# Kernel optimization log

Measured on AMD Instinct MI355X. Metric: run time of the kernel, lower is better.

Reference implementation:

```python
import jax, jax.numpy as jnp
import numpy as np

N_NODES = 100000
N_EDGES = 1600000
D = 128


def setup_inputs() -> dict:
    key = jax.random.key(0)
    ks = jax.random.split(key, 10)
    features = jax.random.normal(ks[0], (N_NODES, D), dtype=jnp.float32)
    edge_index = jax.random.randint(ks[1], (2, N_EDGES), 0, N_NODES, dtype=jnp.int64)
    edge_weight = jax.random.uniform(ks[2], (N_EDGES,), dtype=jnp.float32)
    scale = 1.0 / np.sqrt(D)
    W1 = jax.random.normal(ks[3], (D, D), dtype=jnp.float32) * scale
    b1 = jnp.zeros((D,), dtype=jnp.float32)
    a1 = jnp.full((D,), 0.25, dtype=jnp.float32)  # PReLU init
    W2 = jax.random.normal(ks[4], (D, D), dtype=jnp.float32) * scale
    b2 = jnp.zeros((D,), dtype=jnp.float32)
    a2 = jnp.full((D,), 0.25, dtype=jnp.float32)
    return {"features": features, "edge_index": edge_index, "edge_weight": edge_weight,
            "W1": W1, "b1": b1, "a1": a1, "W2": W2, "b2": b2, "a2": a2}


def _gcn_norm(edge_index, edge_weight, n_nodes):
    # PyG GCNConv default: add self-loops (weight 1), symmetric normalization.
    src, dst = edge_index[0], edge_index[1]
    loop = jnp.arange(n_nodes, dtype=src.dtype)
    src = jnp.concatenate([src, loop])
    dst = jnp.concatenate([dst, loop])
    w = jnp.concatenate([edge_weight, jnp.ones((n_nodes,), edge_weight.dtype)])
    deg = jax.ops.segment_sum(w, dst, num_segments=n_nodes)  # in-degree (target)
    dis = jnp.where(deg > 0, jax.lax.rsqrt(deg), 0.0)
    norm = dis[src] * w * dis[dst]  # [E + N]
    return src, dst, norm


def _gcn_layer(x, W, b, src, dst, norm, n_nodes):
    h = x @ W                                 # [N, D] dense GEMM first (PyG order)
    msg = h[src] * norm[:, None]              # gather + scale, [E+N, D]
    out = jax.ops.segment_sum(msg, dst, num_segments=n_nodes)
    return out + b


def _prelu(x, a):
    return jnp.where(x >= 0, x, a * x)


def reference(features, edge_index, edge_weight, W1, b1, a1, W2, b2, a2):
    n = features.shape[0]
    src, dst, norm = _gcn_norm(edge_index, edge_weight, n)
    # dropout is identity in eval mode
    x = _prelu(_gcn_layer(features, W1, b1, src, dst, norm, n), a1)
    x = _prelu(_gcn_layer(x, W2, b2, src, dst, norm, n), a2)
    return x
```

## Files before the change

### kernel.cpp

```cpp
#include <hip/hip_runtime.h>
#include <cstdint>

#define NN 100000
#define NE 1600000
#define DD 128
#define NB 250
#define BSZ 400
#define NHB ((NE + 8191) / 8192)

typedef unsigned int uint;
typedef unsigned short ushort;
typedef unsigned long long u64;

typedef __attribute__((ext_vector_type(8))) short short8;
typedef __attribute__((ext_vector_type(4))) float floatx4;

__device__ inline uint f2bf(float f) {
    uint u = __float_as_uint(f);
    return (u + 0x7fffu + ((u >> 16) & 1u)) >> 16;
}


__global__ __launch_bounds__(256) void bucket_hist(const int* __restrict__ dst,
                                                   uint* __restrict__ bcp) {
    __shared__ uint h[NB];
    int tid = threadIdx.x;
    if (tid < NB) h[tid] = 0u;
    __syncthreads();
    int e0 = blockIdx.x * 8192 + tid;
#pragma unroll
    for (int k = 0; k < 32; ++k) {
        int e = e0 + 256 * k;
        if (e < NE) atomicAdd(&h[(uint)dst[e] / BSZ], 1u);
    }
    __syncthreads();
    if (tid < NB) bcp[blockIdx.x * 256 + tid] = h[tid];
}

__global__ __launch_bounds__(256) void bucket_prefix(const uint* __restrict__ bcp,
                                                     uint* __restrict__ bbase,
                                                     uint* __restrict__ bcur) {
    __shared__ uint cnt[NB];
    int tid = threadIdx.x;
    if (tid < NB) {
        uint s = 0;
        for (int j = 0; j < NHB; ++j) s += bcp[j * 256 + tid];
        cnt[tid] = s;
    }
    __syncthreads();
    int lane = tid;
    if (lane < 64) {
        uint v[4], s = 0;
#pragma unroll
        for (int k = 0; k < 4; ++k) {
            int i = lane * 4 + k;
            v[k] = (i < NB) ? cnt[i] : 0u;
            s += v[k];
        }
        uint inc = s;
#pragma unroll
        for (int d = 1; d < 64; d <<= 1) {
            uint t = __shfl_up(inc, (unsigned)d, 64);
            if (lane >= d) inc += t;
        }
        uint run = inc - s;
#pragma unroll
        for (int k = 0; k < 4; ++k) {
            int i = lane * 4 + k;
            if (i < NB) { bbase[i] = run; bcur[i] = run; run += v[k]; }
        }
        if (lane == 63) bbase[NB] = run;
    }
}

__global__ __launch_bounds__(256) void bucket_append(const int* __restrict__ src,
                                                     const int* __restrict__ dst,
                                                     const float* __restrict__ w,
                                                     uint* __restrict__ bcur,
                                                     int2* __restrict__ etmp) {
    __shared__ uint h[NB];
    __shared__ uint res[NB];
    int tid = threadIdx.x;
    if (tid < NB) h[tid] = 0u;
    __syncthreads();
    int e0 = blockIdx.x * 4096 + tid;
    uint rank[16], bkt[16];
#pragma unroll
    for (int k = 0; k < 16; ++k) {
        int e = e0 + 256 * k;
        if (e < NE) {
            uint b = (uint)dst[e] / BSZ;
            bkt[k] = b;
            rank[k] = atomicAdd(&h[b], 1u);
        } else bkt[k] = 0xffffffffu;
    }
    __syncthreads();
    if (tid < NB) res[tid] = h[tid] ? atomicAdd(&bcur[tid], h[tid]) : 0u;
    __syncthreads();
#pragma unroll
    for (int k = 0; k < 16; ++k) {
        if (bkt[k] != 0xffffffffu) {
            int e = e0 + 256 * k;
            uint dl = (uint)dst[e] - bkt[k] * BSZ;
            uint wq = (uint)(w[e] * 8388608.0f);
            if (wq > 8388607u) wq = 8388607u;
            etmp[res[bkt[k]] + rank[k]] = make_int2(src[e], (int)((dl << 23) | wq));
        }
    }
}

__global__ __launch_bounds__(256) void bucket_build(const int2* __restrict__ etmp,
                                                    const uint* __restrict__ bbase,
                                                    float* __restrict__ dis,
                                                    int* __restrict__ hist_g,
                                                    int* __restrict__ rowstart,
                                                    int2* __restrict__ edges) {
    __shared__ u64   wc[BSZ];
    __shared__ uint  cur[BSZ];
    __shared__ float disl[BSZ];
    int tid = threadIdx.x;
    int b = blockIdx.x;
    int n0 = b * BSZ;
    for (int i = tid; i < BSZ; i += 256) wc[i] = 0ull;
    __syncthreads();
    uint base = bbase[b], end = bbase[b + 1];
    for (uint i = base + tid; i < end; i += 256) {
        uint y = (uint)etmp[i].y;
        uint dl = y >> 23;
        atomicAdd(&wc[dl], ((u64)1 << 40) | (u64)(y & 0x7fffffu));
    }
    __syncthreads();
    if (tid < 64) {
        uint v[7], s = 0;
#pragma unroll
        for (int k = 0; k < 7; ++k) {
            int i = tid * 7 + k;
            v[k] = (i < BSZ) ? (uint)(wc[i] >> 40) : 0u;
            s += v[k];
        }
        uint inc = s;
#pragma unroll
        for (int d = 1; d < 64; d <<= 1) {
            uint t = __shfl_up(inc, (unsigned)d, 64);
            if (tid >= d) inc += t;
        }
        uint run = inc - s;
#pragma unroll
        for (int k = 0; k < 7; ++k) {
            int i = tid * 7 + k;
            if (i < BSZ) { cur[i] = run; run += v[k]; }
        }
    }
    __syncthreads();
    for (int i = tid; i < BSZ; i += 256) {
        u64 v = wc[i];
        float wsum = (float)(v & 0xffffffffffull) * (1.0f / 8388608.0f);
        float ds = rsqrtf(1.0f + wsum);
        disl[i] = ds;
        dis[n0 + i] = ds;
        hist_g[n0 + i] = (int)(v >> 40);
        rowstart[n0 + i] = (int)(base + cur[i]);
    }
    __syncthreads();
    for (uint i = base + tid; i < end; i += 256) {
        int2 e = etmp[i];
        uint y = (uint)e.y;
        uint dl = y >> 23;
        float wv = (float)(y & 0x7fffffu) * (1.0f / 8388608.0f);
        uint p = atomicAdd(&cur[dl], 1u);
        float nrm = wv * disl[dl];
        edges[base + p] = make_int2(e.x, __float_as_int(nrm));
    }
}

#define WTS 136
#define NTILES ((NN + 63) / 64)

template <bool AF32>
__global__ __launch_bounds__(256) void gemm_mfma(const void* __restrict__ Xv,
                                                 const float* __restrict__ W,
                                                 const float* __restrict__ dis,
                                                 ushort* __restrict__ HB) {
    __shared__ ushort Wt[DD * WTS];
    int tid = threadIdx.x;
#pragma unroll
    for (int it = 0; it < 16; ++it) {
        int flat = (tid + it * 256) * 4;
        int k = flat >> 7, n = flat & 127;
        float4 wv = *(const float4*)&W[flat];
        Wt[(n + 0) * WTS + k] = (ushort)f2bf(wv.x);
        Wt[(n + 1) * WTS + k] = (ushort)f2bf(wv.y);
        Wt[(n + 2) * WTS + k] = (ushort)f2bf(wv.z);
        Wt[(n + 3) * WTS + k] = (ushort)f2bf(wv.w);
    }
    __syncthreads();

    int wave = tid >> 6, lane = tid & 63;
    int q = lane >> 4, l16 = lane & 15;

    for (int tile = blockIdx.x; tile < NTILES; tile += gridDim.x) {
        int row0 = tile * 64 + wave * 16;

        int arow = row0 + l16;
        if (arow >= NN) arow = NN - 1;
        short8 afr[4];
        if (AF32) {
            const float* xr = (const float*)Xv + (size_t)arow * DD + q * 8;
#pragma unroll
            for (int ks = 0; ks < 4; ++ks) {
                float4 f0 = *(const float4*)(xr + ks * 32);
                float4 f1 = *(const float4*)(xr + ks * 32 + 4);
                uint4 u;
                u.x = f2bf(f0.x) | (f2bf(f0.y) << 16);
                u.y = f2bf(f0.z) | (f2bf(f0.w) << 16);
                u.z = f2bf(f1.x) | (f2bf(f1.y) << 16);
                u.w = f2bf(f1.z) | (f2bf(f1.w) << 16);
                afr[ks] = __builtin_bit_cast(short8, u);
            }
        } else {
            const ushort* xr = (const ushort*)Xv + (size_t)arow * DD + q * 8;
#pragma unroll
            for (int ks = 0; ks < 4; ++ks)
                afr[ks] = *(const short8*)(xr + ks * 32);
        }

        floatx4 acc[8];
#pragma unroll
        for (int ct = 0; ct < 8; ++ct) acc[ct] = (floatx4)(0.0f);

#pragma unroll
        for (int ct = 0; ct < 8; ++ct) {
            const ushort* wp = &Wt[(ct * 16 + l16) * WTS + q * 8];
#pragma unroll
            for (int ks = 0; ks < 4; ++ks) {
                short8 bfr = *(const short8*)(wp + ks * 32);
                acc[ct] = __builtin_amdgcn_mfma_f32_16x16x32_bf16(afr[ks], bfr, acc[ct], 0, 0, 0);
            }
        }

#pragma unroll
        for (int reg = 0; reg < 4; ++reg) {
            int r = row0 + q * 4 + reg;
            if (r < NN) {
                float ds = dis[r];
                ushort* orow = HB + (size_t)r * DD + l16;
#pragma unroll
                for (int ct = 0; ct < 8; ++ct)
                    orow[ct * 16] = (ushort)f2bf(acc[ct][reg] * ds);
            }
        }
    }
}

template <bool BF16OUT>
__global__ __launch_bounds__(256) void gather_finalize(const ushort* __restrict__ hb,
                                                       const int2* __restrict__ edges,
                                                       const int* __restrict__ rowstart,
                                                       const int* __restrict__ hist,
                                                       const float* __restrict__ dis,
                                                       const float* __restrict__ b,
                                                       const float* __restrict__ a,
                                                       void* __restrict__ xout) {
    int wid = __builtin_amdgcn_readfirstlane(threadIdx.x >> 6);
    int lane = threadIdx.x & 63;
    int nodeA = blockIdx.x * 8 + wid * 2;
    int nodeB = nodeA + 1;
    uint lane4 = (uint)lane * 4u;
    const char* hbase = (const char*)hb;

    int rsA  = rowstart[nodeA];
    int rsB  = rowstart[nodeB];
    int cntA = hist[nodeA];
    int cntB = hist[nodeB];
    float dsA = dis[nodeA];
    float dsB = dis[nodeB];
    const int2* epA = edges + rsA;
    const int2* epB = edges + rsB;

    uint suA = *(const uint*)(hbase + ((size_t)(uint)nodeA << 8) + lane4);
    uint suB = *(const uint*)(hbase + ((size_t)(uint)nodeB << 8) + lane4);
    float2 a0, a1, a2, a3, b0, b1, b2, b3;
    a0.x = __uint_as_float(suA << 16) * dsA;
    a0.y = __uint_as_float(suA & 0xffff0000u) * dsA;
    b0.x = __uint_as_float(suB << 16) * dsB;
    b0.y = __uint_as_float(suB & 0xffff0000u) * dsB;
    a1 = make_float2(0.f, 0.f); a2 = a1; a3 = a1;
    b1 = a1; b2 = a1; b3 = a1;

    int nbA = (cntA + 15) >> 4;
    int nbB = (cntB + 15) >> 4;
    int nb = nbA > nbB ? nbA : nbB;

    for (int t = 0; t < nb; ++t) {
        int remA = cntA - t * 16;
        int remB = cntB - t * 16;
        int2 eA[16], eB[16];
#pragma unroll
        for (int k = 0; k < 16; ++k) eA[k] = epA[t * 16 + k];
#pragma unroll
        for (int k = 0; k < 16; ++k) eB[k] = epB[t * 16 + k];

        uint gA[16], gB[16];
        float nA[16], nB[16];
#pragma unroll
        for (int k = 0; k < 16; ++k) {
            bool live = k < remA;
            uint s = live ? (uint)eA[k].x : 0u;
            nA[k] = live ? __int_as_float(eA[k].y) : 0.0f;
            gA[k] = *(const uint*)(hbase + ((size_t)s << 8) + lane4);
        }
#pragma unroll
        for (int k = 0; k < 16; ++k) {
            bool live = k < remB;
            uint s = live ? (uint)eB[k].x : 0u;
            nB[k] = live ? __int_as_float(eB[k].y) : 0.0f;
            gB[k] = *(const uint*)(hbase + ((size_t)s << 8) + lane4);
        }
#pragma unroll
        for (int k = 0; k < 16; ++k) {
            float2* ac = (k & 3) == 0 ? &a0 : (k & 3) == 1 ? &a1 : (k & 3) == 2 ? &a2 : &a3;
            ac->x += __uint_as_float(gA[k] << 16) * nA[k];
            ac->y += __uint_as_float(gA[k] & 0xffff0000u) * nA[k];
        }
#pragma unroll
        for (int k = 0; k < 16; ++k) {
            float2* ac = (k & 3) == 0 ? &b0 : (k & 3) == 1 ? &b1 : (k & 3) == 2 ? &b2 : &b3;
            ac->x += __uint_as_float(gB[k] << 16) * nB[k];
            ac->y += __uint_as_float(gB[k] & 0xffff0000u) * nB[k];
        }
    }

    float2 bb = ((const float2*)b)[lane];
    float2 aa = ((const float2*)a)[lane];
    float rA0 = a0.x + a1.x + a2.x + a3.x + bb.x;
    float rA1 = a0.y + a1.y + a2.y + a3.y + bb.y;
    float rB0 = b0.x + b1.x + b2.x + b3.x + bb.x;
    float rB1 = b0.y + b1.y + b2.y + b3.y + bb.y;
    rA0 = rA0 >= 0.f ? rA0 : aa.x * rA0;
    rA1 = rA1 >= 0.f ? rA1 : aa.y * rA1;
    rB0 = rB0 >= 0.f ? rB0 : aa.x * rB0;
    rB1 = rB1 >= 0.f ? rB1 : aa.y * rB1;
    if (BF16OUT) {
        ((uint*)xout)[(size_t)nodeA * 64 + lane] = f2bf(rA0) | (f2bf(rA1) << 16);
        ((uint*)xout)[(size_t)nodeB * 64 + lane] = f2bf(rB0) | (f2bf(rB1) << 16);
    } else {
        float2 oA; oA.x = rA0; oA.y = rA1;
        float2 oB; oB.x = rB0; oB.y = rB1;
        ((float2*)xout)[(size_t)nodeA * 64 + lane] = oA;
        ((float2*)xout)[(size_t)nodeB * 64 + lane] = oB;
    }
}

extern "C" void kernel_launch(void* const* d_in, const int* in_sizes, int n_in,
                              void* d_out, int out_size, void* d_ws, size_t ws_size,
                              hipStream_t stream) {
    const float* feat = (const float*)d_in[0];
    const int*   ei   = (const int*)d_in[1];
    const float* ew   = (const float*)d_in[2];
    const float* W1   = (const float*)d_in[3];
    const float* b1   = (const float*)d_in[4];
    const float* a1   = (const float*)d_in[5];
    const float* W2   = (const float*)d_in[6];
    const float* b2   = (const float*)d_in[7];
    const float* a2   = (const float*)d_in[8];
    float* out = (float*)d_out;

    const int* srcp = ei;
    const int* dstp = ei + NE;

    char* wsb = (char*)d_ws;
    size_t off = 0;
    uint* bcp    = (uint*)(wsb + off); off += 4ull * 256 * NHB;
    uint* bbase  = (uint*)(wsb + off); off += 4096;
    uint* bcur   = (uint*)(wsb + off); off += 4096;
    float* dis   = (float*)(wsb + off); off += 4ull * NN;
    int* hist    = (int*)(wsb + off); off += 4ull * NN;
    int* rowstart= (int*)(wsb + off); off += 4ull * NN;
    int2* etmp   = (int2*)(wsb + off); off += 8ull * NE;
    int2* edges  = (int2*)(wsb + off); off += 8ull * NE;
    ushort* hb   = (ushort*)(wsb + off); off += 2ull * NN * DD;
    ushort* x1b  = (ushort*)(wsb + off); off += 2ull * NN * DD;

    bucket_hist<<<NHB, 256, 0, stream>>>(dstp, bcp);
    bucket_prefix<<<1, 256, 0, stream>>>(bcp, bbase, bcur);
    bucket_append<<<(NE + 4095) / 4096, 256, 0, stream>>>(srcp, dstp, ew, bcur, etmp);
    bucket_build<<<NB, 256, 0, stream>>>(etmp, bbase, dis, hist, rowstart, edges);

    const int gemm_blocks = (NTILES + 1) / 2;
    const int gath_blocks = NN / 8;

    gemm_mfma<true><<<gemm_blocks, 256, 0, stream>>>(feat, W1, dis, hb);
    gather_finalize<true><<<gath_blocks, 256, 0, stream>>>(hb, edges, rowstart, hist, dis, b1, a1, x1b);
    gemm_mfma<false><<<gemm_blocks, 256, 0, stream>>>(x1b, W2, dis, hb);
    gather_finalize<false><<<gath_blocks, 256, 0, stream>>>(hb, edges, rowstart, hist, dis, b2, a2, out);
}
```

Measured before the change: 368.9 us.

## Fuse all stages into one persistent cooperative kernel with grid syncs

Replaces the eight separate launches (bucket histogram, prefix, append, build, two GEMMs, two gathers) with one cooperative persistent kernel that uses grid-wide syncs between phases. Weight transpose and bf16 conversion move to a first phase in global memory so GEMM blocks only copy them into LDS. The aim is to remove launch gaps and per-kernel ramp-up and tail. In exchange the grid is capped by occupancy, so the gather phase gets far fewer resident blocks than before, and grid.sync barriers add their own cost.

```diff
diff --git a/kernel.cpp b/kernel.cpp
--- a/kernel.cpp
+++ b/kernel.cpp
@@ -1,12 +1,17 @@
 #include <hip/hip_runtime.h>
+#include <hip/hip_cooperative_groups.h>
 #include <cstdint>
+
+namespace cg = cooperative_groups;
 
 #define NN 100000
 #define NE 1600000
 #define DD 128
 #define NB 250
 #define BSZ 400
-#define NHB ((NE + 8191) / 8192)
+#define GB 1024
+#define WTS 136
+#define NTILES ((NN + 63) / 64)
 
 typedef unsigned int uint;
 typedef unsigned short ushort;
@@ -14,193 +19,42 @@
 
 typedef __attribute__((ext_vector_type(8))) short short8;
 typedef __attribute__((ext_vector_type(4))) float floatx4;
+
+struct FusedP {
+    const float* feat; const int* srcp; const int* dstp; const float* ew;
+    const float* W1; const float* b1; const float* a1;
+    const float* W2; const float* b2; const float* a2;
+    ushort* wt1; ushort* wt2;
+    uint* bcp; uint* bbase; uint* bcur;
+    float* dis; int* hist; int* rowstart;
+    int2* etmp; int2* edges;
+    ushort* hb; ushort* x1b; float* out;
+};
 
 __device__ inline uint f2bf(float f) {
     uint u = __float_as_uint(f);
     return (u + 0x7fffu + ((u >> 16) & 1u)) >> 16;
 }
 
-
-__global__ __launch_bounds__(256) void bucket_hist(const int* __restrict__ dst,
-                                                   uint* __restrict__ bcp) {
-    __shared__ uint h[NB];
-    int tid = threadIdx.x;
-    if (tid < NB) h[tid] = 0u;
+template <bool AF32>
+__device__ __forceinline__ void gemm_phase(const void* Xv, const ushort* Wtg,
+                                           const float* dis, ushort* HB,
+                                           char* smem, int tid) {
+    ushort* Wt = (ushort*)smem;
+#pragma unroll
+    for (int u = 0; u < 8; ++u) {
+        int unit = tid + u * 256;
+        int n = unit >> 4, c = unit & 15;
+        *(short8*)&Wt[n * WTS + c * 8] = *(const short8*)(Wtg + n * DD + c * 8);
+    }
     __syncthreads();
-    int e0 = blockIdx.x * 8192 + tid;
-#pragma unroll
-    for (int k = 0; k < 32; ++k) {
-        int e = e0 + 256 * k;
-        if (e < NE) atomicAdd(&h[(uint)dst[e] / BSZ], 1u);
-    }
-    __syncthreads();
-    if (tid < NB) bcp[blockIdx.x * 256 + tid] = h[tid];
-}
-
-__global__ __launch_bounds__(256) void bucket_prefix(const uint* __restrict__ bcp,
-                                                     uint* __restrict__ bbase,
-                                                     uint* __restrict__ bcur) {
-    __shared__ uint cnt[NB];
-    int tid = threadIdx.x;
-    if (tid < NB) {
-        uint s = 0;
-        for (int j = 0; j < NHB; ++j) s += bcp[j * 256 + tid];
-        cnt[tid] = s;
-    }
-    __syncthreads();
-    int lane = tid;
-    if (lane < 64) {
-        uint v[4], s = 0;
-#pragma unroll
-        for (int k = 0; k < 4; ++k) {
-            int i = lane * 4 + k;
-            v[k] = (i < NB) ? cnt[i] : 0u;
-            s += v[k];
-        }
-        uint inc = s;
-#pragma unroll
-        for (int d = 1; d < 64; d <<= 1) {
-            uint t = __shfl_up(inc, (unsigned)d, 64);
-            if (lane >= d) inc += t;
-        }
-        uint run = inc - s;
-#pragma unroll
-        for (int k = 0; k < 4; ++k) {
-            int i = lane * 4 + k;
-            if (i < NB) { bbase[i] = run; bcur[i] = run; run += v[k]; }
-        }
-        if (lane == 63) bbase[NB] = run;
-    }
-}
-
-__global__ __launch_bounds__(256) void bucket_append(const int* __restrict__ src,
-                                                     const int* __restrict__ dst,
-                                                     const float* __restrict__ w,
-                                                     uint* __restrict__ bcur,
-                                                     int2* __restrict__ etmp) {
-    __shared__ uint h[NB];
-    __shared__ uint res[NB];
-    int tid = threadIdx.x;
-    if (tid < NB) h[tid] = 0u;
-    __syncthreads();
-    int e0 = blockIdx.x * 4096 + tid;
-    uint rank[16], bkt[16];
-#pragma unroll
-    for (int k = 0; k < 16; ++k) {
-        int e = e0 + 256 * k;
-        if (e < NE) {
-            uint b = (uint)dst[e] / BSZ;
-            bkt[k] = b;
-            rank[k] = atomicAdd(&h[b], 1u);
-        } else bkt[k] = 0xffffffffu;
-    }
-    __syncthreads();
-    if (tid < NB) res[tid] = h[tid] ? atomicAdd(&bcur[tid], h[tid]) : 0u;
-    __syncthreads();
-#pragma unroll
-    for (int k = 0; k < 16; ++k) {
-        if (bkt[k] != 0xffffffffu) {
-            int e = e0 + 256 * k;
-            uint dl = (uint)dst[e] - bkt[k] * BSZ;
-            uint wq = (uint)(w[e] * 8388608.0f);
-            if (wq > 8388607u) wq = 8388607u;
-            etmp[res[bkt[k]] + rank[k]] = make_int2(src[e], (int)((dl << 23) | wq));
-        }
-    }
-}
-
-__global__ __launch_bounds__(256) void bucket_build(const int2* __restrict__ etmp,
-                                                    const uint* __restrict__ bbase,
-                                                    float* __restrict__ dis,
-                                                    int* __restrict__ hist_g,
-                                                    int* __restrict__ rowstart,
-                                                    int2* __restrict__ edges) {
-    __shared__ u64   wc[BSZ];
-    __shared__ uint  cur[BSZ];
-    __shared__ float disl[BSZ];
-    int tid = threadIdx.x;
-    int b = blockIdx.x;
-    int n0 = b * BSZ;
-    for (int i = tid; i < BSZ; i += 256) wc[i] = 0ull;
-    __syncthreads();
-    uint base = bbase[b], end = bbase[b + 1];
-    for (uint i = base + tid; i < end; i += 256) {
-        uint y = (uint)etmp[i].y;
-        uint dl = y >> 23;
-        atomicAdd(&wc[dl], ((u64)1 << 40) | (u64)(y & 0x7fffffu));
-    }
-    __syncthreads();
-    if (tid < 64) {
-        uint v[7], s = 0;
-#pragma unroll
-        for (int k = 0; k < 7; ++k) {
-            int i = tid * 7 + k;
-            v[k] = (i < BSZ) ? (uint)(wc[i] >> 40) : 0u;
-            s += v[k];
-        }
-        uint inc = s;
-#pragma unroll
-        for (int d = 1; d < 64; d <<= 1) {
-            uint t = __shfl_up(inc, (unsigned)d, 64);
-            if (tid >= d) inc += t;
-        }
-        uint run = inc - s;
-#pragma unroll
-        for (int k = 0; k < 7; ++k) {
-            int i = tid * 7 + k;
-            if (i < BSZ) { cur[i] = run; run += v[k]; }
-        }
-    }
-    __syncthreads();
-    for (int i = tid; i < BSZ; i += 256) {
-        u64 v = wc[i];
-        float wsum = (float)(v & 0xffffffffffull) * (1.0f / 8388608.0f);
-        float ds = rsqrtf(1.0f + wsum);
-        disl[i] = ds;
-        dis[n0 + i] = ds;
-        hist_g[n0 + i] = (int)(v >> 40);
-        rowstart[n0 + i] = (int)(base + cur[i]);
-    }
-    __syncthreads();
-    for (uint i = base + tid; i < end; i += 256) {
-        int2 e = etmp[i];
-        uint y = (uint)e.y;
-        uint dl = y >> 23;
-        float wv = (float)(y & 0x7fffffu) * (1.0f / 8388608.0f);
-        uint p = atomicAdd(&cur[dl], 1u);
-        float nrm = wv * disl[dl];
-        edges[base + p] = make_int2(e.x, __float_as_int(nrm));
-    }
-}
-
-#define WTS 136
-#define NTILES ((NN + 63) / 64)
-
-template <bool AF32>
-__global__ __launch_bounds__(256) void gemm_mfma(const void* __restrict__ Xv,
-                                                 const float* __restrict__ W,
-                                                 const float* __restrict__ dis,
-                                                 ushort* __restrict__ HB) {
-    __shared__ ushort Wt[DD * WTS];
-    int tid = threadIdx.x;
-#pragma unroll
-    for (int it = 0; it < 16; ++it) {
-        int flat = (tid + it * 256) * 4;
-        int k = flat >> 7, n = flat & 127;
-        float4 wv = *(const float4*)&W[flat];
-        Wt[(n + 0) * WTS + k] = (ushort)f2bf(wv.x);
-        Wt[(n + 1) * WTS + k] = (ushort)f2bf(wv.y);
-        Wt[(n + 2) * WTS + k] = (ushort)f2bf(wv.z);
-        Wt[(n + 3) * WTS + k] = (ushort)f2bf(wv.w);
-    }
-    __syncthreads();
-
-    int wave = tid >> 6, lane = tid & 63;
+
+    int lane = tid & 63;
+    int wave = tid >> 6;
     int q = lane >> 4, l16 = lane & 15;
 
     for (int tile = blockIdx.x; tile < NTILES; tile += gridDim.x) {
         int row0 = tile * 64 + wave * 16;
-
         int arow = row0 + l16;
         if (arow >= NN) arow = NN - 1;
         short8 afr[4];
@@ -250,147 +104,319 @@
             }
         }
     }
+    __syncthreads();
 }
 
 template <bool BF16OUT>
-__global__ __launch_bounds__(256) void gather_finalize(const ushort* __restrict__ hb,
-                                                       const int2* __restrict__ edges,
-                                                       const int* __restrict__ rowstart,
-                                                       const int* __restrict__ hist,
-                                                       const float* __restrict__ dis,
-                                                       const float* __restrict__ b,
-                                                       const float* __restrict__ a,
-                                                       void* __restrict__ xout) {
-    int wid = __builtin_amdgcn_readfirstlane(threadIdx.x >> 6);
-    int lane = threadIdx.x & 63;
-    int nodeA = blockIdx.x * 8 + wid * 2;
-    int nodeB = nodeA + 1;
+__device__ __forceinline__ void gather_phase(const ushort* hb, const int2* edges,
+                                             const int* rowstart, const int* hist,
+                                             const float* dis, const float* bv,
+                                             const float* av, void* xout, int tid) {
+    int wid = __builtin_amdgcn_readfirstlane(tid >> 6);
+    int lane = tid & 63;
     uint lane4 = (uint)lane * 4u;
     const char* hbase = (const char*)hb;
 
-    int rsA  = rowstart[nodeA];
-    int rsB  = rowstart[nodeB];
-    int cntA = hist[nodeA];
-    int cntB = hist[nodeB];
-    float dsA = dis[nodeA];
-    float dsB = dis[nodeB];
-    const int2* epA = edges + rsA;
-    const int2* epB = edges + rsB;
-
-    uint suA = *(const uint*)(hbase + ((size_t)(uint)nodeA << 8) + lane4);
-    uint suB = *(const uint*)(hbase + ((size_t)(uint)nodeB << 8) + lane4);
-    float2 a0, a1, a2, a3, b0, b1, b2, b3;
-    a0.x = __uint_as_float(suA << 16) * dsA;
-    a0.y = __uint_as_float(suA & 0xffff0000u) * dsA;
-    b0.x = __uint_as_float(suB << 16) * dsB;
-    b0.y = __uint_as_float(suB & 0xffff0000u) * dsB;
-    a1 = make_float2(0.f, 0.f); a2 = a1; a3 = a1;
-    b1 = a1; b2 = a1; b3 = a1;
-
-    int nbA = (cntA + 15) >> 4;
-    int nbB = (cntB + 15) >> 4;
-    int nb = nbA > nbB ? nbA : nbB;
-
-    for (int t = 0; t < nb; ++t) {
-        int remA = cntA - t * 16;
-        int remB = cntB - t * 16;
-        int2 eA[16], eB[16];
-#pragma unroll
-        for (int k = 0; k < 16; ++k) eA[k] = epA[t * 16 + k];
-#pragma unroll
-        for (int k = 0; k < 16; ++k) eB[k] = epB[t * 16 + k];
-
-        uint gA[16], gB[16];
-        float nA[16], nB[16];
-#pragma unroll
-        for (int k = 0; k < 16; ++k) {
-            bool live = k < remA;
-            uint s = live ? (uint)eA[k].x : 0u;
-            nA[k] = live ? __int_as_float(eA[k].y) : 0.0f;
-            gA[k] = *(const uint*)(hbase + ((size_t)s << 8) + lane4);
-        }
-#pragma unroll
-        for (int k = 0; k < 16; ++k) {
-            bool live = k < remB;
-            uint s = live ? (uint)eB[k].x : 0u;
-            nB[k] = live ? __int_as_float(eB[k].y) : 0.0f;
-            gB[k] = *(const uint*)(hbase + ((size_t)s << 8) + lane4);
-        }
-#pragma unroll
-        for (int k = 0; k < 16; ++k) {
-            float2* ac = (k & 3) == 0 ? &a0 : (k & 3) == 1 ? &a1 : (k & 3) == 2 ? &a2 : &a3;
-            ac->x += __uint_as_float(gA[k] << 16) * nA[k];
-            ac->y += __uint_as_float(gA[k] & 0xffff0000u) * nA[k];
-        }
-#pragma unroll
-        for (int k = 0; k < 16; ++k) {
-            float2* ac = (k & 3) == 0 ? &b0 : (k & 3) == 1 ? &b1 : (k & 3) == 2 ? &b2 : &b3;
-            ac->x += __uint_as_float(gB[k] << 16) * nB[k];
-            ac->y += __uint_as_float(gB[k] & 0xffff0000u) * nB[k];
-        }
-    }
-
-    float2 bb = ((const float2*)b)[lane];
-    float2 aa = ((const float2*)a)[lane];
-    float rA0 = a0.x + a1.x + a2.x + a3.x + bb.x;
-    float rA1 = a0.y + a1.y + a2.y + a3.y + bb.y;
-    float rB0 = b0.x + b1.x + b2.x + b3.x + bb.x;
-    float rB1 = b0.y + b1.y + b2.y + b3.y + bb.y;
-    rA0 = rA0 >= 0.f ? rA0 : aa.x * rA0;
-    rA1 = rA1 >= 0.f ? rA1 : aa.y * rA1;
-    rB0 = rB0 >= 0.f ? rB0 : aa.x * rB0;
-    rB1 = rB1 >= 0.f ? rB1 : aa.y * rB1;
-    if (BF16OUT) {
-        ((uint*)xout)[(size_t)nodeA * 64 + lane] = f2bf(rA0) | (f2bf(rA1) << 16);
-        ((uint*)xout)[(size_t)nodeB * 64 + lane] = f2bf(rB0) | (f2bf(rB1) << 16);
-    } else {
-        float2 oA; oA.x = rA0; oA.y = rA1;
-        float2 oB; oB.x = rB0; oB.y = rB1;
-        ((float2*)xout)[(size_t)nodeA * 64 + lane] = oA;
-        ((float2*)xout)[(size_t)nodeB * 64 + lane] = oB;
-    }
+    for (int g = blockIdx.x; g < NN / 8; g += gridDim.x) {
+        int nodeA = g * 8 + wid * 2;
+        int nodeB = nodeA + 1;
+
+        int rsA  = rowstart[nodeA];
+        int rsB  = rowstart[nodeB];
+        int cntA = hist[nodeA];
+        int cntB = hist[nodeB];
+        float dsA = dis[nodeA];
+        float dsB = dis[nodeB];
+        const int2* epA = edges + rsA;
+        const int2* epB = edges + rsB;
+
+        uint suA = *(const uint*)(hbase + ((size_t)(uint)nodeA << 8) + lane4);
+        uint suB = *(const uint*)(hbase + ((size_t)(uint)nodeB << 8) + lane4);
+        float2 a0, a1, a2, a3, b0, b1, b2, b3;
+        a0.x = __uint_as_float(suA << 16) * dsA;
+        a0.y = __uint_as_float(suA & 0xffff0000u) * dsA;
+        b0.x = __uint_as_float(suB << 16) * dsB;
+        b0.y = __uint_as_float(suB & 0xffff0000u) * dsB;
+        a1 = make_float2(0.f, 0.f); a2 = a1; a3 = a1;
+        b1 = a1; b2 = a1; b3 = a1;
+
+        int nbA = (cntA + 15) >> 4;
+        int nbB = (cntB + 15) >> 4;
+        int nb = nbA > nbB ? nbA : nbB;
+
+        for (int t = 0; t < nb; ++t) {
+            int remA = cntA - t * 16;
+            int remB = cntB - t * 16;
+            int2 eA[16], eB[16];
+#pragma unroll
+            for (int k = 0; k < 16; ++k) eA[k] = epA[t * 16 + k];
+#pragma unroll
+            for (int k = 0; k < 16; ++k) eB[k] = epB[t * 16 + k];
+
+            uint gA[16], gB[16];
+            float nA[16], nB[16];
+#pragma unroll
+            for (int k = 0; k < 16; ++k) {
+                bool live = k < remA;
+                uint s = live ? (uint)eA[k].x : 0u;
+                nA[k] = live ? __int_as_float(eA[k].y) : 0.0f;
+                gA[k] = *(const uint*)(hbase + ((size_t)s << 8) + lane4);
+            }
+#pragma unroll
+            for (int k = 0; k < 16; ++k) {
+                bool live = k < remB;
+                uint s = live ? (uint)eB[k].x : 0u;
+                nB[k] = live ? __int_as_float(eB[k].y) : 0.0f;
+                gB[k] = *(const uint*)(hbase + ((size_t)s << 8) + lane4);
+            }
+#pragma unroll
+            for (int k = 0; k < 16; ++k) {
+                float2* ac = (k & 3) == 0 ? &a0 : (k & 3) == 1 ? &a1 : (k & 3) == 2 ? &a2 : &a3;
+                ac->x += __uint_as_float(gA[k] << 16) * nA[k];
+                ac->y += __uint_as_float(gA[k] & 0xffff0000u) * nA[k];
+            }
+#pragma unroll
+            for (int k = 0; k < 16; ++k) {
+                float2* ac = (k & 3) == 0 ? &b0 : (k & 3) == 1 ? &b1 : (k & 3) == 2 ? &b2 : &b3;
+                ac->x += __uint_as_float(gB[k] << 16) * nB[k];
+                ac->y += __uint_as_float(gB[k] & 0xffff0000u) * nB[k];
+            }
+        }
+
+        float2 bb = ((const float2*)bv)[lane];
+        float2 aa = ((const float2*)av)[lane];
+        float rA0 = a0.x + a1.x + a2.x + a3.x + bb.x;
+        float rA1 = a0.y + a1.y + a2.y + a3.y + bb.y;
+        float rB0 = b0.x + b1.x + b2.x + b3.x + bb.x;
+        float rB1 = b0.y + b1.y + b2.y + b3.y + bb.y;
+        rA0 = rA0 >= 0.f ? rA0 : aa.x * rA0;
+        rA1 = rA1 >= 0.f ? rA1 : aa.y * rA1;
+        rB0 = rB0 >= 0.f ? rB0 : aa.x * rB0;
+        rB1 = rB1 >= 0.f ? rB1 : aa.y * rB1;
+        if (BF16OUT) {
+            ((uint*)xout)[(size_t)nodeA * 64 + lane] = f2bf(rA0) | (f2bf(rA1) << 16);
+            ((uint*)xout)[(size_t)nodeB * 64 + lane] = f2bf(rB0) | (f2bf(rB1) << 16);
+        } else {
+            float2 oA; oA.x = rA0; oA.y = rA1;
+            float2 oB; oB.x = rB0; oB.y = rB1;
+            ((float2*)xout)[(size_t)nodeA * 64 + lane] = oA;
+            ((float2*)xout)[(size_t)nodeB * 64 + lane] = oB;
+        }
+    }
+}
+
+__global__ __launch_bounds__(256, 4) void fused_all(FusedP p) {
+    __shared__ __align__(16) char smem[DD * WTS * 2];
+    int tid = threadIdx.x;
+    cg::grid_group grid = cg::this_grid();
+
+    for (int i = blockIdx.x * 256 + tid; i < DD * DD; i += gridDim.x * 256) {
+        int k = i >> 7, n = i & 127;
+        p.wt1[n * DD + k] = (ushort)f2bf(p.W1[i]);
+        p.wt2[n * DD + k] = (ushort)f2bf(p.W2[i]);
+    }
+    {
+        uint* h = (uint*)smem;
+        if (tid < NB) h[tid] = 0u;
+        __syncthreads();
+        for (int e = blockIdx.x * 256 + tid; e < NE; e += gridDim.x * 256)
+            atomicAdd(&h[(uint)p.dstp[e] / BSZ], 1u);
+        __syncthreads();
+        if (tid < NB) p.bcp[(size_t)tid * GB + blockIdx.x] = h[tid];
+    }
+    __threadfence();
+    grid.sync();
+
+    if (blockIdx.x == 0) {
+        uint* cnt = (uint*)smem;
+        if (tid < NB) {
+            const uint4* q4 = (const uint4*)(p.bcp + (size_t)tid * GB);
+            uint s = 0;
+            int nj = gridDim.x >> 2;
+            for (int j = 0; j < nj; ++j) { uint4 v = q4[j]; s += v.x + v.y + v.z + v.w; }
+            cnt[tid] = s;
+        }
+        __syncthreads();
+        if (tid < 64) {
+            uint v[4], s = 0;
+#pragma unroll
+            for (int k = 0; k < 4; ++k) {
+                int i = tid * 4 + k;
+                v[k] = (i < NB) ? cnt[i] : 0u;
+                s += v[k];
+            }
+            uint inc = s;
+#pragma unroll
+            for (int d = 1; d < 64; d <<= 1) {
+                uint t = __shfl_up(inc, (unsigned)d, 64);
+                if (tid >= d) inc += t;
+            }
+            uint run = inc - s;
+#pragma unroll
+            for (int k = 0; k < 4; ++k) {
+                int i = tid * 4 + k;
+                if (i < NB) { p.bbase[i] = run; p.bcur[i] = run; run += v[k]; }
+            }
+            if (tid == 63) p.bbase[NB] = run;
+        }
+    }
+    __threadfence();
+    grid.sync();
+
+    {
+        uint* h = (uint*)smem;
+        uint* res = (uint*)smem + 256;
+        for (int e0b = blockIdx.x * 4096; e0b < NE; e0b += gridDim.x * 4096) {
+            if (tid < NB) h[tid] = 0u;
+            __syncthreads();
+            int e0 = e0b + tid;
+            uint rank[16], bkt[16];
+#pragma unroll
+            for (int k = 0; k < 16; ++k) {
+                int e = e0 + 256 * k;
+                if (e < NE) {
+                    uint bk = (uint)p.dstp[e] / BSZ;
+                    bkt[k] = bk;
+                    rank[k] = atomicAdd(&h[bk], 1u);
+                } else bkt[k] = 0xffffffffu;
+            }
+            __syncthreads();
+            if (tid < NB) res[tid] = h[tid] ? atomicAdd(&p.bcur[tid], h[tid]) : 0u;
+            __syncthreads();
+#pragma unroll
+            for (int k = 0; k < 16; ++k) {
+                if (bkt[k] != 0xffffffffu) {
+                    int e = e0 + 256 * k;
+                    uint dl = (uint)p.dstp[e] - bkt[k] * BSZ;
+                    uint wq = (uint)(p.ew[e] * 8388608.0f);
+                    if (wq > 8388607u) wq = 8388607u;
+                    p.etmp[res[bkt[k]] + rank[k]] = make_int2(p.srcp[e], (int)((dl << 23) | wq));
+                }
+            }
+            __syncthreads();
+        }
+    }
+    __threadfence();
+    grid.sync();
+
+    {
+        u64*   wc   = (u64*)smem;
+        uint*  curq = (uint*)(smem + BSZ * 8);
+        float* disl = (float*)(smem + BSZ * 8 + BSZ * 4);
+        for (int b = blockIdx.x; b < NB; b += gridDim.x) {
+            int n0 = b * BSZ;
+            for (int i = tid; i < BSZ; i += 256) wc[i] = 0ull;
+            __syncthreads();
+            uint base = p.bbase[b], end = p.bbase[b + 1];
+            for (uint i = base + tid; i < end; i += 256) {
+                uint y = (uint)p.etmp[i].y;
+                atomicAdd(&wc[y >> 23], ((u64)1 << 40) | (u64)(y & 0x7fffffu));
+            }
+            __syncthreads();
+            if (tid < 64) {
+                uint v[7], s = 0;
+#pragma unroll
+                for (int k = 0; k < 7; ++k) {
+                    int i = tid * 7 + k;
+                    v[k] = (i < BSZ) ? (uint)(wc[i] >> 40) : 0u;
+                    s += v[k];
+                }
+                uint inc = s;
+#pragma unroll
+                for (int d = 1; d < 64; d <<= 1) {
+                    uint t = __shfl_up(inc, (unsigned)d, 64);
+                    if (tid >= d) inc += t;
+                }
+                uint run = inc - s;
+#pragma unroll
+                for (int k = 0; k < 7; ++k) {
+                    int i = tid * 7 + k;
+                    if (i < BSZ) { curq[i] = run; run += v[k]; }
+                }
+            }
+            __syncthreads();
+            for (int i = tid; i < BSZ; i += 256) {
+                u64 v = wc[i];
+                float wsum = (float)(v & 0xffffffffffull) * (1.0f / 8388608.0f);
+                float dsv = rsqrtf(1.0f + wsum);
+                disl[i] = dsv;
+                p.dis[n0 + i] = dsv;
+                p.hist[n0 + i] = (int)(v >> 40);
+                p.rowstart[n0 + i] = (int)(base + curq[i]);
+            }
+            __syncthreads();
+            for (uint i = base + tid; i < end; i += 256) {
+                int2 e = p.etmp[i];
+                uint y = (uint)e.y;
+                uint dl = y >> 23;
+                float wv = (float)(y & 0x7fffffu) * (1.0f / 8388608.0f);
+                uint pos = atomicAdd(&curq[dl], 1u);
+                p.edges[base + pos] = make_int2(e.x, __float_as_int(wv * disl[dl]));
+            }
+            __syncthreads();
+        }
+    }
+    __threadfence();
+    grid.sync();
+
+    gemm_phase<true>(p.feat, p.wt1, p.dis, p.hb, smem, tid);
+    __threadfence();
+    grid.sync();
+
+    gather_phase<true>(p.hb, p.edges, p.rowstart, p.hist, p.dis, p.b1, p.a1, p.x1b, tid);
+    __threadfence();
+    grid.sync();
+
+    gemm_phase<false>(p.x1b, p.wt2, p.dis, p.hb, smem, tid);
+    __threadfence();
+    grid.sync();
+
+    gather_phase<false>(p.hb, p.edges, p.rowstart, p.hist, p.dis, p.b2, p.a2, p.out, tid);
 }
 
 extern "C" void kernel_launch(void* const* d_in, const int* in_sizes, int n_in,
                               void* d_out, int out_size, void* d_ws, size_t ws_size,
                               hipStream_t stream) {
-    const float* feat = (const float*)d_in[0];
-    const int*   ei   = (const int*)d_in[1];
-    const float* ew   = (const float*)d_in[2];
-    const float* W1   = (const float*)d_in[3];
-    const float* b1   = (const float*)d_in[4];
-    const float* a1   = (const float*)d_in[5];
-    const float* W2   = (const float*)d_in[6];
-    const float* b2   = (const float*)d_in[7];
-    const float* a2   = (const float*)d_in[8];
-    float* out = (float*)d_out;
-
-    const int* srcp = ei;
-    const int* dstp = ei + NE;
-
     char* wsb = (char*)d_ws;
     size_t off = 0;
-    uint* bcp    = (uint*)(wsb + off); off += 4ull * 256 * NHB;
-    uint* bbase  = (uint*)(wsb + off); off += 4096;
-    uint* bcur   = (uint*)(wsb + off); off += 4096;
-    float* dis   = (float*)(wsb + off); off += 4ull * NN;
-    int* hist    = (int*)(wsb + off); off += 4ull * NN;
-    int* rowstart= (int*)(wsb + off); off += 4ull * NN;
-    int2* etmp   = (int2*)(wsb + off); off += 8ull * NE;
-    int2* edges  = (int2*)(wsb + off); off += 8ull * NE;
-    ushort* hb   = (ushort*)(wsb + off); off += 2ull * NN * DD;
-    ushort* x1b  = (ushort*)(wsb + off); off += 2ull * NN * DD;
-
-    bucket_hist<<<NHB, 256, 0, stream>>>(dstp, bcp);
-    bucket_prefix<<<1, 256, 0, stream>>>(bcp, bbase, bcur);
-    bucket_append<<<(NE + 4095) / 4096, 256, 0, stream>>>(srcp, dstp, ew, bcur, etmp);
-    bucket_build<<<NB, 256, 0, stream>>>(etmp, bbase, dis, hist, rowstart, edges);
-
-    const int gemm_blocks = (NTILES + 1) / 2;
-    const int gath_blocks = NN / 8;
-
-    gemm_mfma<true><<<gemm_blocks, 256, 0, stream>>>(feat, W1, dis, hb);
-    gather_finalize<true><<<gath_blocks, 256, 0, stream>>>(hb, edges, rowstart, hist, dis, b1, a1, x1b);
-    gemm_mfma<false><<<gemm_blocks, 256, 0, stream>>>(x1b, W2, dis, hb);
-    gather_finalize<false><<<gath_blocks, 256, 0, stream>>>(hb, edges, rowstart, hist, dis, b2, a2, out);
+    uint* bcp     = (uint*)(wsb + off); off += 4ull * NB * GB;
+    ushort* wt1   = (ushort*)(wsb + off); off += 2ull * DD * DD;
+    ushort* wt2   = (ushort*)(wsb + off); off += 2ull * DD * DD;
+    uint* bbase   = (uint*)(wsb + off); off += 4096;
+    uint* bcur    = (uint*)(wsb + off); off += 4096;
+    float* dis    = (float*)(wsb + off); off += 4ull * NN;
+    int* hist     = (int*)(wsb + off); off += 4ull * NN;
+    int* rowstart = (int*)(wsb + off); off += 4ull * NN;
+    int2* etmp    = (int2*)(wsb + off); off += 8ull * NE;
+    int2* edges   = (int2*)(wsb + off); off += 8ull * NE;
+    ushort* hb    = (ushort*)(wsb + off); off += 2ull * NN * DD;
+    ushort* x1b   = (ushort*)(wsb + off); off += 2ull * NN * DD;
+
+    FusedP p;
+    p.feat = (const float*)d_in[0];
+    p.srcp = (const int*)d_in[1];
+    p.dstp = (const int*)d_in[1] + NE;
+    p.ew   = (const float*)d_in[2];
+    p.W1 = (const float*)d_in[3]; p.b1 = (const float*)d_in[4]; p.a1 = (const float*)d_in[5];
+    p.W2 = (const float*)d_in[6]; p.b2 = (const float*)d_in[7]; p.a2 = (const float*)d_in[8];
+    p.wt1 = wt1; p.wt2 = wt2;
+    p.bcp = bcp; p.bbase = bbase; p.bcur = bcur;
+    p.dis = dis; p.hist = hist; p.rowstart = rowstart;
+    p.etmp = etmp; p.edges = edges;
+    p.hb = hb; p.x1b = x1b;
+    p.out = (float*)d_out;
+
+    static int gblocks = 0;
+    if (gblocks == 0) {
+        int nb = 0;
+        hipOccupancyMaxActiveBlocksPerMultiprocessor(&nb, fused_all, 256, 0);
+        int g = nb * 256;
+        if (g > GB) g = GB;
+        if (g < 256) g = 256;
+        gblocks = g;
+    }
+
+    void* kp[] = { (void*)&p };
+    hipLaunchCooperativeKernel((const void*)fused_all, dim3(gblocks), dim3(256),
+                               kp, 0, stream);
 }
```

Measured after the change: 1.286 ms. 3.49x slower.
